# Kernel tuning notes

Hardware: AMD Instinct MI355X
Metric: run time of the kernel (lower is better)

The kernel has to match this reference:

```python
import jax, jax.numpy as jnp
import numpy as np

S, B, E = 4096, 2, 1024
H = 8
WIN = 256  # one-sided window w; band width = 2*w+1


def _band_scores(q, k_pad, seq_len, band):
    # q: (B,S,H,D), k_pad: (B,S+2w,H,D). Returns (B,S,H,band) banded QK^T.
    def f(o):
        ks = jax.lax.dynamic_slice_in_dim(k_pad, o, seq_len, axis=1)
        return jnp.einsum('bshd,bshd->bsh', q, ks)
    s = jax.lax.map(f, jnp.arange(band))  # (band,B,S,H)
    return jnp.moveaxis(s, 0, -1)          # (B,S,H,band)


def _band_av(probs, v_pad, seq_len, band):
    # probs: (B,S,H,band), v_pad: (B,S+2w,H,D) zero-padded (out-of-range keys
    # contribute zero vectors, matching diagonaled_mm's internal masking).
    bsz, _, heads, _ = probs.shape
    d = v_pad.shape[-1]
    def body(carry, o):
        vs = jax.lax.dynamic_slice_in_dim(v_pad, o, seq_len, axis=1)
        p = jax.lax.dynamic_slice_in_dim(probs, o, 1, axis=3)  # (B,S,H,1)
        return carry + p * vs, None
    init = jnp.zeros((bsz, seq_len, heads, d), probs.dtype)
    out, _ = jax.lax.scan(body, init, jnp.arange(band))
    return out


def setup_inputs() -> dict:
    key = jax.random.key(0)
    ks = jax.random.split(key, 7)
    val = jax.random.normal(ks[0], (S, B, E), dtype=jnp.float32)
    Wq = jax.random.normal(ks[1], (E, E), dtype=jnp.float32) * 0.02
    bq = jax.random.normal(ks[2], (E,), dtype=jnp.float32) * 0.02
    Wk = jax.random.normal(ks[3], (E, E), dtype=jnp.float32) * 0.02
    bk = jax.random.normal(ks[4], (E,), dtype=jnp.float32) * 0.02
    Wv = jax.random.normal(ks[5], (E, E), dtype=jnp.float32) * 0.02
    bv = jax.random.normal(ks[6], (E,), dtype=jnp.float32) * 0.02
    return {"val": val, "Wq": Wq, "bq": bq, "Wk": Wk, "bk": bk, "Wv": Wv, "bv": bv}


def reference(val, Wq, bq, Wk, bk, Wv, bv):
    seq_len, bsz, embed = val.shape
    heads, w = H, WIN
    d = embed // heads
    band = 2 * w + 1
    x = jnp.swapaxes(val, 0, 1)  # (B,S,E), matches val.transpose(0,1)
    scale = 1.0 / np.sqrt(d)
    q = (x @ Wq.T + bq) * scale
    k = x @ Wk.T + bk
    v = x @ Wv.T + bv
    # Faithful to torch: .view(seq_len, bsz, H, D) on a (bsz, seq_len, E)
    # contiguous tensor reinterprets memory (a scramble when B != S), then
    # transpose(0,1). jnp.reshape on row-major matches torch .view exactly.
    mq = jnp.swapaxes(q.reshape(seq_len, bsz, heads, d), 0, 1)  # (B,S,H,D)
    mk = jnp.swapaxes(k.reshape(seq_len, bsz, heads, d), 0, 1)
    mv = jnp.swapaxes(v.reshape(seq_len, bsz, heads, d), 0, 1)
    k_pad = jnp.pad(mk, ((0, 0), (w, w), (0, 0), (0, 0)))  # zero pad => padding=0 scores
    v_pad = jnp.pad(mv, ((0, 0), (w, w), (0, 0), (0, 0)))
    scores = _band_scores(mq, k_pad, seq_len, band)  # (B,S,H,2w+1)
    # No masking before softmax (faithful: padding=0 entries enter softmax as 0)
    probs = jax.nn.softmax(scores, axis=-1)
    # dropout in eval mode (training=False) is identity
    attn = _band_av(probs, v_pad, seq_len, band)  # (B,S,H,D)
    out = jnp.swapaxes(attn, 0, 1).reshape(seq_len, bsz, embed)
    return out
```

## Files before the change

### kernel.cpp

```cpp
#include <hip/hip_runtime.h>
#include <stdint.h>

#define SEQ   4096
#define EMB   1024
#define HD    128
#define WIN   256
#define MROWS 8192

typedef unsigned short u16;
typedef unsigned long long u64;
typedef __bf16 v8bf  __attribute__((ext_vector_type(8)));
typedef float  v4f   __attribute__((ext_vector_type(4)));
typedef u16    v8u16 __attribute__((ext_vector_type(8)));

__device__ __forceinline__ u16 f2bf(float f) {
  uint32_t u = __builtin_bit_cast(uint32_t, f);
  u += 0x7FFFu + ((u >> 16) & 1u);
  return (u16)(u >> 16);
}
__device__ __forceinline__ void gl_lds16(const u16* g, u16* l) {
  __builtin_amdgcn_global_load_lds((const __attribute__((address_space(1))) void*)g,
                                   (__attribute__((address_space(3))) void*)l,
                                   16, 0, 0);
}

__global__ __launch_bounds__(256)
void cvt_f32_bf16(const float* __restrict__ val,
                  const float* __restrict__ Wq,
                  const float* __restrict__ Wk,
                  const float* __restrict__ Wv,
                  u16* __restrict__ valbf, u16* __restrict__ Wbf)
{
  const int seg = blockIdx.y;
  const float* src; u16* dst; int nblk;
  if (seg == 0)      { src = val; dst = valbf;              nblk = 4096; }
  else if (seg == 1) { src = Wq;  dst = Wbf;                nblk = 512;  }
  else if (seg == 2) { src = Wk;  dst = Wbf + (1u << 20);   nblk = 512;  }
  else               { src = Wv;  dst = Wbf + (2u << 20);   nblk = 512;  }
  if ((int)blockIdx.x >= nblk) return;
  const int t = blockIdx.x * 256 + threadIdx.x;
  float4 a = ((const float4*)src)[2 * t];
  float4 b = ((const float4*)src)[2 * t + 1];
  v8u16 o;
  o[0] = f2bf(a.x); o[1] = f2bf(a.y); o[2] = f2bf(a.z); o[3] = f2bf(a.w);
  o[4] = f2bf(b.x); o[5] = f2bf(b.y); o[6] = f2bf(b.z); o[7] = f2bf(b.w);
  ((v8u16*)dst)[t] = o;
}

__global__ __launch_bounds__(256, 3)
void qkv_gemm(const u16* __restrict__ valbf, const u16* __restrict__ Wbf,
              const float* __restrict__ bq, const float* __restrict__ bk,
              const float* __restrict__ bv,
              u16* __restrict__ Qb, u16* __restrict__ Kb, u16* __restrict__ VTg)
{
  __shared__ __align__(16) u16 As[128 * 64];
  __shared__ __align__(16) u16 Bs[128 * 64];

  const int tid  = threadIdx.x;
  const int lane = tid & 63;
  const int w    = tid >> 6;
  const int quad = lane >> 4;
  const int lq   = lane & 15;
  const int wm   = w >> 1, wn = w & 1;

  const int bm = blockIdx.x;
  const int bn = blockIdx.y;

  const int seg = bn >> 3;
  const u16*   Wsel = Wbf + (size_t)seg * EMB * EMB;
  const float* bsel = seg == 0 ? bq : (seg == 1 ? bk : bv);
  const int nseg0 = (bn & 7) * 128;

  const u16* arow[4];
  const u16* brow[4];
#pragma unroll
  for (int call = 0; call < 4; ++call) {
    int c  = call * 256 + w * 64 + lane;
    int m  = c >> 3;
    int qs = c & 7;
    int q  = qs ^ (m & 7);
    int a2 = bm * 128 + m;
    int aa = 2 * (a2 & 4095) + (a2 >> 12);
    int grow = (aa & 4095) * 2 + (aa >> 12);
    arow[call] = valbf + (size_t)grow * EMB + q * 8;
    int n = nseg0 + m;
    brow[call] = Wsel + (size_t)n * EMB + q * 8;
  }

  v4f acc[4][4];
#pragma unroll
  for (int mt = 0; mt < 4; ++mt)
#pragma unroll
    for (int nt = 0; nt < 4; ++nt) acc[mt][nt] = (v4f){0.f, 0.f, 0.f, 0.f};

#pragma unroll 1
  for (int kt = 0; kt < 16; ++kt) {
    const int k0 = kt * 64;
    __syncthreads();
#pragma unroll
    for (int call = 0; call < 4; ++call) {
      gl_lds16(arow[call] + k0, &As[(call * 256 + w * 64) * 8]);
      gl_lds16(brow[call] + k0, &Bs[(call * 256 + w * 64) * 8]);
    }
    __syncthreads();
#pragma unroll
    for (int ks = 0; ks < 2; ++ks) {
      v8bf afr[4], bfr[4];
      const int qa = ks * 4 + quad;
#pragma unroll
      for (int mt = 0; mt < 4; ++mt) {
        int m = wm * 64 + mt * 16 + lq;
        afr[mt] = *(const v8bf*)&As[(m * 8 + (qa ^ (m & 7))) * 8];
      }
#pragma unroll
      for (int nt = 0; nt < 4; ++nt) {
        int n = wn * 64 + nt * 16 + lq;
        bfr[nt] = *(const v8bf*)&Bs[(n * 8 + (qa ^ (n & 7))) * 8];
      }
#pragma unroll
      for (int mt = 0; mt < 4; ++mt)
#pragma unroll
        for (int nt = 0; nt < 4; ++nt)
          acc[mt][nt] = __builtin_amdgcn_mfma_f32_16x16x32_bf16(afr[mt], bfr[nt], acc[mt][nt], 0, 0, 0);
    }
  }

  const float scale = 0.08838834764831845f;
  float bias[4];
#pragma unroll
  for (int nt = 0; nt < 4; ++nt)
    bias[nt] = bsel[nseg0 + wn * 64 + nt * 16 + lq];

  if (seg == 2) {
    const int h  = bn & 7;
    const int bp = bm >> 5;
    const int s0 = (bm & 31) * 128;
#pragma unroll
    for (int mt = 0; mt < 4; ++mt) {
      int mb = wm * 64 + mt * 16 + quad * 4;
#pragma unroll
      for (int nt = 0; nt < 4; ++nt) {
        int n = wn * 64 + nt * 16 + lq;
        u64 pk = 0;
#pragma unroll
        for (int r = 0; r < 4; ++r)
          pk |= (u64)f2bf(acc[mt][nt][r] + bias[nt]) << (16 * r);
        *(u64*)&VTg[((size_t)(bp * 8 + h) * HD + n) * SEQ + s0 + mb] = pk;
      }
    }
  } else {
    u16* Osel = (seg == 0) ? Qb : Kb;
#pragma unroll
    for (int mt = 0; mt < 4; ++mt) {
      int rbase = bm * 128 + wm * 64 + mt * 16 + quad * 4;
#pragma unroll
      for (int nt = 0; nt < 4; ++nt) {
        int ncol = nseg0 + wn * 64 + nt * 16 + lq;
#pragma unroll
        for (int r = 0; r < 4; ++r) {
          float v = acc[mt][nt][r] + bias[nt];
          if (seg == 0) v *= scale;
          Osel[(size_t)(rbase + r) * EMB + ncol] = f2bf(v);
        }
      }
    }
  }
}

__global__ __launch_bounds__(256, 2)
void local_attn(const u16* __restrict__ Qb, const u16* __restrict__ Kb,
                const u16* __restrict__ VTg, float* __restrict__ out)
{
  __shared__ __align__(16) u16 sK [2][64 * 128];
  __shared__ __align__(16) u16 sVT[2][128 * 64];
  __shared__ __align__(16) u16 sP [4][16 * 72];

  const int tid  = threadIdx.x;
  const int lane = tid & 63;
  const int w    = tid >> 6;
  const int quad = lane >> 4;
  const int lq   = lane & 15;

  const int bh = blockIdx.x;
  const int q0 = blockIdx.y * 128;
  const int bp = bh >> 3;
  const int h  = bh & 7;
  const size_t rowbase = (size_t)bp * SEQ;

  const u16* Kbase = Kb + rowbase * EMB + h * HD;
  const u16* Vbase = VTg + (size_t)bh * HD * SEQ;

  v8bf qf[2][4];
#pragma unroll
  for (int mt = 0; mt < 2; ++mt) {
    const u16* qrow = Qb + (rowbase + q0 + w * 32 + mt * 16 + lq) * EMB + h * HD;
#pragma unroll
    for (int ks = 0; ks < 4; ++ks)
      qf[mt][ks] = *(const v8bf*)(qrow + ks * 32 + quad * 8);
  }

  v4f oacc[2][8];
#pragma unroll
  for (int mt = 0; mt < 2; ++mt)
#pragma unroll
    for (int dt = 0; dt < 8; ++dt) oacc[mt][dt] = (v4f){0.f, 0.f, 0.f, 0.f};
  float ls[2][4] = {{0.f,0.f,0.f,0.f},{0.f,0.f,0.f,0.f}};

  const int jlo = (q0 - WIN > 0) ? q0 - WIN : 0;
  const int jhi = (q0 + 128 + WIN < SEQ) ? q0 + 128 + WIN : SEQ;
  const int nit = (jhi - jlo) >> 6;

  auto stage = [&](int kb, int p) {
#pragma unroll
    for (int call = 0; call < 4; ++call) {
      int s = call * 256 + w * 64 + lane;
      int row = s >> 4, sl = s & 15;
      int q = sl ^ (row & 15);
      gl_lds16(Kbase + (size_t)(kb + row) * EMB + q * 8,
               &sK[p][(call * 256 + w * 64) * 8]);
    }
#pragma unroll
    for (int call = 0; call < 4; ++call) {
      int s = call * 256 + w * 64 + lane;
      int d = s >> 3, sl = s & 7;
      int q = sl ^ (d & 7);
      gl_lds16(Vbase + (size_t)d * SEQ + kb + q * 8,
               &sVT[p][(call * 256 + w * 64) * 8]);
    }
  };

  stage(jlo, 0);

#pragma unroll 1
  for (int it = 0; it < nit; ++it) {
    const int p  = it & 1;
    const int kb = jlo + it * 64;
    __syncthreads();
    if (it + 1 < nit) stage(kb + 64, p ^ 1);

    v8bf vf[2][8];
#pragma unroll
    for (int kv = 0; kv < 2; ++kv)
#pragma unroll
      for (int dt = 0; dt < 8; ++dt) {
        int d = dt * 16 + lq;
        vf[kv][dt] = *(const v8bf*)&sVT[p][(d * 8 + ((kv * 4 + quad) ^ (d & 7))) * 8];
      }

    v4f sfr[2][4];
#pragma unroll
    for (int mt = 0; mt < 2; ++mt)
#pragma unroll
      for (int nt = 0; nt < 4; ++nt) sfr[mt][nt] = (v4f){0.f, 0.f, 0.f, 0.f};
#pragma unroll
    for (int ks = 0; ks < 4; ++ks) {
      const int sl = (ks * 4 + quad) ^ lq;
#pragma unroll
      for (int nt = 0; nt < 4; ++nt) {
        v8bf kf = *(const v8bf*)&sK[p][((nt * 16 + lq) * 16 + sl) * 8];
        sfr[0][nt] = __builtin_amdgcn_mfma_f32_16x16x32_bf16(qf[0][ks], kf, sfr[0][nt], 0, 0, 0);
        sfr[1][nt] = __builtin_amdgcn_mfma_f32_16x16x32_bf16(qf[1][ks], kf, sfr[1][nt], 0, 0, 0);
      }
    }

    const bool need_mask = (kb <= q0 - 192) || (kb >= q0 + 256);
#pragma unroll
    for (int mt = 0; mt < 2; ++mt) {
#pragma unroll
      for (int nt = 0; nt < 4; ++nt) {
#pragma unroll
        for (int r = 0; r < 4; ++r) {
          float pv = __expf(sfr[mt][nt][r]);
          if (need_mask) {
            int j  = kb + nt * 16 + lq;
            int sr = q0 + w * 32 + mt * 16 + quad * 4 + r;
            int dd = j - sr;
            pv = (dd <= WIN && dd >= -WIN) ? pv : 0.f;
          }
          ls[mt][r] += pv;
          sP[w][(quad * 4 + r) * 72 + nt * 16 + lq] = f2bf(pv);
        }
      }
#pragma unroll
      for (int kv = 0; kv < 2; ++kv) {
        v8bf pf = *(const v8bf*)&sP[w][lq * 72 + kv * 32 + quad * 8];
#pragma unroll
        for (int dt = 0; dt < 8; ++dt)
          oacc[mt][dt] = __builtin_amdgcn_mfma_f32_16x16x32_bf16(pf, vf[kv][dt], oacc[mt][dt], 0, 0, 0);
      }
    }
  }

#pragma unroll
  for (int mt = 0; mt < 2; ++mt) {
    float lrow[4];
#pragma unroll
    for (int r = 0; r < 4; ++r) {
      float t = ls[mt][r];
#pragma unroll
      for (int off = 1; off < 16; off <<= 1) t += __shfl_xor(t, off);
      int sr = q0 + w * 32 + mt * 16 + quad * 4 + r;
      int npl = WIN - sr;             if (npl < 0) npl = 0;
      int npr = sr - (SEQ - 1 - WIN); if (npr < 0) npr = 0;
      lrow[r] = t + (float)(npl + npr);
    }
#pragma unroll
    for (int dt = 0; dt < 8; ++dt) {
#pragma unroll
      for (int r = 0; r < 4; ++r) {
        int sr = q0 + w * 32 + mt * 16 + quad * 4 + r;
        out[(size_t)(2 * sr + bp) * EMB + h * HD + dt * 16 + lq] = oacc[mt][dt][r] / lrow[r];
      }
    }
  }
}

extern "C" void kernel_launch(void* const* d_in, const int* in_sizes, int n_in,
                              void* d_out, int out_size, void* d_ws, size_t ws_size,
                              hipStream_t stream) {
  const float* val = (const float*)d_in[0];
  const float* bq  = (const float*)d_in[2];
  const float* bk  = (const float*)d_in[4];
  const float* bv  = (const float*)d_in[6];
  float* out = (float*)d_out;

  u16* valbf = (u16*)d_ws;
  u16* Wbf   = valbf + (size_t)MROWS * EMB;
  u16* Qb    = Wbf + (size_t)3 * EMB * EMB;
  u16* Kb    = Qb + (size_t)MROWS * EMB;
  u16* VTg   = Kb + (size_t)MROWS * EMB;

  hipLaunchKernelGGL(cvt_f32_bf16, dim3(4096, 4), dim3(256), 0, stream,
                     val, (const float*)d_in[1], (const float*)d_in[3],
                     (const float*)d_in[5], valbf, Wbf);
  hipLaunchKernelGGL(qkv_gemm, dim3(64, 24), dim3(256), 0, stream,
                     valbf, Wbf, bq, bk, bv, Qb, Kb, VTg);
  hipLaunchKernelGGL(local_attn, dim3(16, 32), dim3(256), 0, stream,
                     Qb, Kb, VTg, out);
}
```

Baseline: 191.0 us.

## Compute transposed scores to keep P in registers and skip LDS round-trip

Swaps the QK^T MFMA operands so each lane holds scores for one query row, which lets the probabilities feed the PV MFMA (16x16x16 bf16 via inline asm) directly from registers instead of staging through a shared-memory P buffer. The output accumulator becomes transposed, so the row-sum reduction shrinks to two shuffles and results are written as 16-byte vector stores. It removes LDS writes and reads plus their latency, but adds hand-placed s_nop hazards in asm. The mask-skip condition is also changed.

```diff
diff --git a/kernel.cpp b/kernel.cpp
--- a/kernel.cpp
+++ b/kernel.cpp
@@ -12,6 +12,12 @@
 typedef __bf16 v8bf  __attribute__((ext_vector_type(8)));
 typedef float  v4f   __attribute__((ext_vector_type(4)));
 typedef u16    v8u16 __attribute__((ext_vector_type(8)));
+typedef short  v4ss  __attribute__((ext_vector_type(4)));
+
+__device__ __forceinline__ void mfma16(v4f& c, v4ss a, v4ss b) {
+  asm("s_nop 1\n\tv_mfma_f32_16x16x16_bf16 %0, %1, %2, %0"
+      : "+v"(c) : "v"(a), "v"(b));
+}
 
 __device__ __forceinline__ u16 f2bf(float f) {
   uint32_t u = __builtin_bit_cast(uint32_t, f);
@@ -173,7 +179,6 @@
 {
   __shared__ __align__(16) u16 sK [2][64 * 128];
   __shared__ __align__(16) u16 sVT[2][128 * 64];
-  __shared__ __align__(16) u16 sP [4][16 * 72];
 
   const int tid  = threadIdx.x;
   const int lane = tid & 63;
@@ -199,12 +204,12 @@
       qf[mt][ks] = *(const v8bf*)(qrow + ks * 32 + quad * 8);
   }
 
-  v4f oacc[2][8];
+  v4f oaccT[2][8];
 #pragma unroll
   for (int mt = 0; mt < 2; ++mt)
 #pragma unroll
-    for (int dt = 0; dt < 8; ++dt) oacc[mt][dt] = (v4f){0.f, 0.f, 0.f, 0.f};
-  float ls[2][4] = {{0.f,0.f,0.f,0.f},{0.f,0.f,0.f,0.f}};
+    for (int dt = 0; dt < 8; ++dt) oaccT[mt][dt] = (v4f){0.f, 0.f, 0.f, 0.f};
+  float ls0 = 0.f, ls1 = 0.f;
 
   const int jlo = (q0 - WIN > 0) ? q0 - WIN : 0;
   const int jhi = (q0 + 128 + WIN < SEQ) ? q0 + 128 + WIN : SEQ;
@@ -238,79 +243,74 @@
     __syncthreads();
     if (it + 1 < nit) stage(kb + 64, p ^ 1);
 
-    v8bf vf[2][8];
-#pragma unroll
-    for (int kv = 0; kv < 2; ++kv)
-#pragma unroll
-      for (int dt = 0; dt < 8; ++dt) {
-        int d = dt * 16 + lq;
-        vf[kv][dt] = *(const v8bf*)&sVT[p][(d * 8 + ((kv * 4 + quad) ^ (d & 7))) * 8];
-      }
-
-    v4f sfr[2][4];
+    v4f st[2][4];
 #pragma unroll
     for (int mt = 0; mt < 2; ++mt)
 #pragma unroll
-      for (int nt = 0; nt < 4; ++nt) sfr[mt][nt] = (v4f){0.f, 0.f, 0.f, 0.f};
+      for (int nt = 0; nt < 4; ++nt) st[mt][nt] = (v4f){0.f, 0.f, 0.f, 0.f};
 #pragma unroll
     for (int ks = 0; ks < 4; ++ks) {
       const int sl = (ks * 4 + quad) ^ lq;
 #pragma unroll
       for (int nt = 0; nt < 4; ++nt) {
         v8bf kf = *(const v8bf*)&sK[p][((nt * 16 + lq) * 16 + sl) * 8];
-        sfr[0][nt] = __builtin_amdgcn_mfma_f32_16x16x32_bf16(qf[0][ks], kf, sfr[0][nt], 0, 0, 0);
-        sfr[1][nt] = __builtin_amdgcn_mfma_f32_16x16x32_bf16(qf[1][ks], kf, sfr[1][nt], 0, 0, 0);
-      }
-    }
-
-    const bool need_mask = (kb <= q0 - 192) || (kb >= q0 + 256);
+        st[0][nt] = __builtin_amdgcn_mfma_f32_16x16x32_bf16(kf, qf[0][ks], st[0][nt], 0, 0, 0);
+        st[1][nt] = __builtin_amdgcn_mfma_f32_16x16x32_bf16(kf, qf[1][ks], st[1][nt], 0, 0, 0);
+      }
+    }
+
+    const bool need_mask = (kb < q0 - 129) || (kb > q0 + 193);
+    v4ss pf[2][4];
 #pragma unroll
     for (int mt = 0; mt < 2; ++mt) {
 #pragma unroll
       for (int nt = 0; nt < 4; ++nt) {
 #pragma unroll
         for (int r = 0; r < 4; ++r) {
-          float pv = __expf(sfr[mt][nt][r]);
+          float pv = __expf(st[mt][nt][r]);
           if (need_mask) {
-            int j  = kb + nt * 16 + lq;
-            int sr = q0 + w * 32 + mt * 16 + quad * 4 + r;
+            int j  = kb + nt * 16 + quad * 4 + r;
+            int sr = q0 + w * 32 + mt * 16 + lq;
             int dd = j - sr;
             pv = (dd <= WIN && dd >= -WIN) ? pv : 0.f;
           }
-          ls[mt][r] += pv;
-          sP[w][(quad * 4 + r) * 72 + nt * 16 + lq] = f2bf(pv);
+          if (mt == 0) ls0 += pv; else ls1 += pv;
+          pf[mt][nt][r] = (short)f2bf(pv);
         }
       }
-#pragma unroll
-      for (int kv = 0; kv < 2; ++kv) {
-        v8bf pf = *(const v8bf*)&sP[w][lq * 72 + kv * 32 + quad * 8];
-#pragma unroll
-        for (int dt = 0; dt < 8; ++dt)
-          oacc[mt][dt] = __builtin_amdgcn_mfma_f32_16x16x32_bf16(pf, vf[kv][dt], oacc[mt][dt], 0, 0, 0);
-      }
-    }
-  }
+    }
+
+#pragma unroll
+    for (int nt = 0; nt < 4; ++nt) {
+#pragma unroll
+      for (int dt = 0; dt < 8; ++dt) {
+        int d = dt * 16 + lq;
+        int slot = (nt * 2 + (quad >> 1)) ^ (d & 7);
+        v4ss vt = *(const v4ss*)&sVT[p][(d * 8 + slot) * 8 + (quad & 1) * 4];
+        mfma16(oaccT[0][dt], vt, pf[0][nt]);
+        mfma16(oaccT[1][dt], vt, pf[1][nt]);
+      }
+    }
+  }
+
+  asm volatile("s_nop 7\n\ts_nop 7");
 
 #pragma unroll
   for (int mt = 0; mt < 2; ++mt) {
-    float lrow[4];
-#pragma unroll
-    for (int r = 0; r < 4; ++r) {
-      float t = ls[mt][r];
-#pragma unroll
-      for (int off = 1; off < 16; off <<= 1) t += __shfl_xor(t, off);
-      int sr = q0 + w * 32 + mt * 16 + quad * 4 + r;
-      int npl = WIN - sr;             if (npl < 0) npl = 0;
-      int npr = sr - (SEQ - 1 - WIN); if (npr < 0) npr = 0;
-      lrow[r] = t + (float)(npl + npr);
-    }
+    float t = (mt == 0) ? ls0 : ls1;
+    t += __shfl_xor(t, 16);
+    t += __shfl_xor(t, 32);
+    const int sr = q0 + w * 32 + mt * 16 + lq;
+    int npl = WIN - sr;             if (npl < 0) npl = 0;
+    int npr = sr - (SEQ - 1 - WIN); if (npr < 0) npr = 0;
+    const float inv = 1.0f / (t + (float)(npl + npr));
+    float* orow = out + (size_t)(2 * sr + bp) * EMB + h * HD;
 #pragma unroll
     for (int dt = 0; dt < 8; ++dt) {
-#pragma unroll
-      for (int r = 0; r < 4; ++r) {
-        int sr = q0 + w * 32 + mt * 16 + quad * 4 + r;
-        out[(size_t)(2 * sr + bp) * EMB + h * HD + dt * 16 + lq] = oacc[mt][dt][r] / lrow[r];
-      }
+      v4f o;
+#pragma unroll
+      for (int r = 0; r < 4; ++r) o[r] = oaccT[mt][dt][r] * inv;
+      *(v4f*)(orow + dt * 16 + quad * 4) = o;
     }
   }
 }
```

Measured after the change: 188.2 us. No clear change (-1.5%).
